# Kernel tuning notes

Hardware: AMD Instinct MI355X
Metric: run time of the kernel (lower is better)

The kernel has to match this reference:

```python
import jax, jax.numpy as jnp
import numpy as np
from jax import lax

T, IN, OUT, E, R = 32768, 2048, 768, 64, 16
SCALING = 32.0 / 16.0  # lora_alpha / r


def setup_inputs() -> dict:
    key = jax.random.key(0)
    k1, k2, k3, k4 = jax.random.split(key, 4)
    x = jax.random.normal(k1, (T, IN), dtype=jnp.float32)
    # Ragged per-expert token counts summing exactly to T (tokens pre-sorted by expert).
    rng = np.random.default_rng(0)
    m_sizes = jnp.asarray(np.bincount(rng.integers(0, E, size=T), minlength=E), dtype=jnp.int32)
    w_base = jax.random.normal(k2, (E, IN, OUT), dtype=jnp.float32) * 0.02
    # NOTE: original inits lora_B to zeros; we use small random values so the
    # LoRA path contributes non-trivially for correctness testing.
    w_a = jax.random.normal(k3, (E, IN, R), dtype=jnp.float32) * (1.0 / np.sqrt(IN))
    w_b = jax.random.normal(k4, (E, R, OUT), dtype=jnp.float32) * 0.02
    return {"x": x, "m_sizes": m_sizes, "w_base": w_base, "w_a": w_a, "w_b": w_b}


def reference(x, m_sizes, w_base, w_a, w_b):
    # Grouped (ragged) GEMM: rows of x are grouped by expert with sizes m_sizes.
    y = lax.ragged_dot(x, w_base, m_sizes)          # [T, OUT] base path
    a = lax.ragged_dot(x, w_a, m_sizes)             # [T, R]   lora_A
    delta = lax.ragged_dot(a, w_b, m_sizes)         # [T, OUT] lora_B
    return y + delta * SCALING
```

## Files before the change

### kernel.cpp

```cpp
#include <hip/hip_runtime.h>

#define TDIM 32768
#define KDIM 2048
#define NDIM 768
#define EDIM 64
#define RDIM 16
#define SCALE 2.0f

#define BM 128
#define BN 128
#define BKE 64
#define PK 40
#define MAXMT 320

typedef __bf16 bf16;
typedef __attribute__((ext_vector_type(8))) __bf16 bf16x8;
typedef __attribute__((ext_vector_type(4))) __bf16 bf16x4;
typedef __attribute__((ext_vector_type(4))) float f32x4;

#define GLOAD16(gp, lp) \
    __builtin_amdgcn_global_load_lds((const __attribute__((address_space(1))) void*)(gp), \
                                     (__attribute__((address_space(3))) void*)(lp), 16, 0, 0)

__global__ __launch_bounds__(256)
void conv_x_k(const float* __restrict__ x, bf16* __restrict__ xb)
{
    size_t i = ((size_t)blockIdx.x * 256 + threadIdx.x) * 8;
    float4 f0 = *reinterpret_cast<const float4*>(x + i);
    float4 f1 = *reinterpret_cast<const float4*>(x + i + 4);
    bf16x8 v;
    v[0] = (bf16)f0.x; v[1] = (bf16)f0.y; v[2] = (bf16)f0.z; v[3] = (bf16)f0.w;
    v[4] = (bf16)f1.x; v[5] = (bf16)f1.y; v[6] = (bf16)f1.z; v[7] = (bf16)f1.w;
    *reinterpret_cast<bf16x8*>(xb + i) = v;
}

__global__ __launch_bounds__(256)
void conv_w_k(const float* __restrict__ w, bf16* __restrict__ wT)
{
    __shared__ bf16 t[32][65];
    const int e  = blockIdx.z;
    const int n0 = blockIdx.x * 32;
    const int k0 = blockIdx.y * 64;
    const float* src = w + (size_t)e * KDIM * NDIM;
    #pragma unroll
    for (int i = 0; i < 8; ++i) {
        int lin = threadIdx.x + i * 256;
        int k = lin >> 5;
        int c = lin & 31;
        t[c][k] = (bf16)src[(size_t)(k0 + k) * NDIM + n0 + c];
    }
    __syncthreads();
    bf16* dst = wT + ((size_t)e * NDIM + n0) * KDIM + k0;
    #pragma unroll
    for (int i = 0; i < 8; ++i) {
        int lin = threadIdx.x + i * 256;
        int n = lin >> 6;
        int k = lin & 63;
        dst[(size_t)n * KDIM + k] = t[n][k];
    }
}

__global__ __launch_bounds__(256)
void prep_small_k(const float* __restrict__ w_a, const int* __restrict__ m_sizes,
                  bf16* __restrict__ waT, int4* __restrict__ tinfo)
{
    if (blockIdx.x < 16) {
        __shared__ bf16 t[RDIM][132];
        const int e  = blockIdx.y;
        const int k0 = blockIdx.x * 128;
        const float* src = w_a + ((size_t)e * KDIM + k0) * RDIM;
        #pragma unroll
        for (int i = 0; i < 8; ++i) {
            int lin = threadIdx.x + i * 256;
            int k = lin >> 4, r = lin & 15;
            t[r][k] = (bf16)src[lin];
        }
        __syncthreads();
        bf16* dst = waT + (size_t)e * RDIM * KDIM + k0;
        #pragma unroll
        for (int i = 0; i < 8; ++i) {
            int lin = threadIdx.x + i * 256;
            int r = lin >> 7, k = lin & 127;
            dst[(size_t)r * KDIM + k] = t[r][k];
        }
    } else if (blockIdx.y == 0) {
        for (int i = threadIdx.x; i < MAXMT; i += 256)
            tinfo[i] = make_int4(0, 0, 0, 0);
        __syncthreads();
        if (threadIdx.x < 64) {
            const int lane = threadIdx.x;
            int m  = m_sizes[lane];
            int nt = (m + BM - 1) >> 7;
            int pm = m, pt = nt;
            #pragma unroll
            for (int d = 1; d < 64; d <<= 1) {
                int vm = __shfl_up(pm, d);
                int vt = __shfl_up(pt, d);
                if (lane >= d) { pm += vm; pt += vt; }
            }
            int row0 = pm - m, tb = pt - nt;
            for (int tI = 0; tI < nt; ++tI) {
                int rr = m - (tI << 7); if (rr > BM) rr = BM;
                tinfo[tb + tI] = make_int4(lane, row0 + (tI << 7), rr, 0);
            }
        }
    }
}

__global__ __launch_bounds__(256, 2)
void lora_moe_bf16(const bf16* __restrict__ xb,
                   const bf16* __restrict__ wT,
                   const bf16* __restrict__ waT,
                   const float* __restrict__ w_b,
                   const int4* __restrict__ tinfo,
                   float* __restrict__ out)
{
    __shared__ bf16 As[BM][BKE];
    __shared__ bf16 Bs[BN][BKE];
    __shared__ bf16 WaS[RDIM][BKE];

    const int tid  = threadIdx.x;
    const int lane = tid & 63;
    const int wave = tid >> 6;
    const int wm   = wave >> 1;
    const int wn   = wave & 1;
    const int quad = lane >> 4;
    const int lrow = lane & 15;

    const int4 ti = tinfo[blockIdx.y];
    const int rows = ti.z;
    if (rows == 0) return;
    const int e      = ti.x;
    const int tstart = ti.y;
    const int n0     = blockIdx.x * BN;

    const bf16* a_base  = xb  + (size_t)tstart * KDIM;
    const bf16* b_base  = wT  + ((size_t)e * NDIM + n0) * KDIM;
    const bf16* wa_base = waT + (size_t)e * RDIM * KDIM;
    const float* wbb_e  = w_b + (size_t)e * RDIM * NDIM;

    f32x4 acc[4][4];
    f32x4 accA[4];
    #pragma unroll
    for (int i = 0; i < 4; ++i) {
        accA[i] = (f32x4){0.f, 0.f, 0.f, 0.f};
        #pragma unroll
        for (int j = 0; j < 4; ++j) acc[i][j] = (f32x4){0.f, 0.f, 0.f, 0.f};
    }

    const int lr8 = lane >> 3;
    const int lg  = lane & 7;

    const bf16* agp[4];
    const bf16* bgp[4];
    #pragma unroll
    for (int i = 0; i < 4; ++i) {
        int r  = wave * 32 + i * 8 + lr8;
        int gr = r < rows ? r : rows - 1;
        agp[i] = a_base + (size_t)gr * KDIM + ((lg ^ (r & 7)) << 3);
        bgp[i] = b_base + (size_t)r  * KDIM + ((lg ^ (r & 7)) << 3);
    }
    const bf16* wagp = wa_base + (size_t)(wave * 8 + lr8) * KDIM + ((lg ^ lr8) << 3);

    const int swzr = (lrow & 7) << 4;

    for (int kk = 0; kk < KDIM; kk += BKE) {
        __syncthreads();
        #pragma unroll
        for (int i = 0; i < 4; ++i)
            GLOAD16(agp[i], &As[wave * 32 + i * 8][0]);
        #pragma unroll
        for (int i = 0; i < 4; ++i)
            GLOAD16(bgp[i], &Bs[wave * 32 + i * 8][0]);
        if (wave < 2)
            GLOAD16(wagp, &WaS[wave * 8][0]);
        #pragma unroll
        for (int i = 0; i < 4; ++i) { agp[i] += BKE; bgp[i] += BKE; }
        wagp += BKE;
        __syncthreads();

        #pragma unroll
        for (int kh = 0; kh < 2; ++kh) {
            const int cb = (kh * 64 + quad * 16) ^ swzr;
            bf16x8 af[4];
            #pragma unroll
            for (int i = 0; i < 4; ++i)
                af[i] = *reinterpret_cast<const bf16x8*>(
                            (const char*)&As[wm * 64 + i * 16 + lrow][0] + cb);
            bf16x8 wf = *reinterpret_cast<const bf16x8*>(
                            (const char*)&WaS[lrow][0] + cb);
            #pragma unroll
            for (int j = 0; j < 4; ++j) {
                bf16x8 bfr = *reinterpret_cast<const bf16x8*>(
                                 (const char*)&Bs[wn * 64 + j * 16 + lrow][0] + cb);
                #pragma unroll
                for (int i = 0; i < 4; ++i)
                    acc[i][j] = __builtin_amdgcn_mfma_f32_16x16x32_bf16(af[i], bfr, acc[i][j], 0, 0, 0);
            }
            #pragma unroll
            for (int i = 0; i < 4; ++i)
                accA[i] = __builtin_amdgcn_mfma_f32_16x16x32_bf16(af[i], wf, accA[i], 0, 0, 0);
        }
    }

    __syncthreads();
    if (wn == 0) {
        #pragma unroll
        for (int i = 0; i < 4; ++i) {
            int mrow = wm * 64 + i * 16 + quad * 4;
            #pragma unroll
            for (int r = 0; r < 4; ++r) {
                int row = mrow + r;
                char* p = (char*)&As[row][0] + ((lrow * 2) ^ ((row & 7) << 4));
                *reinterpret_cast<bf16*>(p) = (bf16)(accA[i][r] * SCALE);
            }
        }
    } else {
        #pragma unroll
        for (int i = 0; i < 4; ++i) {
            int mrow = wm * 64 + i * 16 + quad * 4;
            #pragma unroll
            for (int r = 0; r < 4; ++r) {
                int row = mrow + r;
                char* p = (char*)&As[row][0] + ((32 + lrow * 2) ^ ((row & 7) << 4));
                *reinterpret_cast<bf16*>(p) = (bf16)0.f;
            }
        }
    }
    {
        int n  = tid & 127;
        int r0 = (tid >> 7) * 8;
        const float* p = wbb_e + (size_t)r0 * NDIM + n0 + n;
        bf16x8 v;
        #pragma unroll
        for (int u = 0; u < 8; ++u) v[u] = (bf16)p[(size_t)u * NDIM];
        char* q = (char*)&Bs[n][0];
        *reinterpret_cast<bf16x8*>(q + ((r0 * 2) ^ ((n & 7) << 4))) = v;
        bf16x8 z = {};
        *reinterpret_cast<bf16x8*>(q + ((32 + r0 * 2) ^ ((n & 7) << 4))) = z;
    }
    __syncthreads();
    #pragma unroll
    for (int i = 0; i < 4; ++i) {
        const int cb2 = (quad * 16) ^ swzr;
        bf16x8 af2 = *reinterpret_cast<const bf16x8*>(
                         (const char*)&As[wm * 64 + i * 16 + lrow][0] + cb2);
        #pragma unroll
        for (int j = 0; j < 4; ++j) {
            bf16x8 bf2 = *reinterpret_cast<const bf16x8*>(
                             (const char*)&Bs[wn * 64 + j * 16 + lrow][0] + cb2);
            acc[i][j] = __builtin_amdgcn_mfma_f32_16x16x32_bf16(af2, bf2, acc[i][j], 0, 0, 0);
        }
    }

    #pragma unroll
    for (int i = 0; i < 4; ++i) {
        int mbase = wm * 64 + i * 16 + quad * 4;
        #pragma unroll
        for (int j = 0; j < 4; ++j) {
            int col = n0 + wn * 64 + j * 16 + lrow;
            #pragma unroll
            for (int r = 0; r < 4; ++r) {
                int mr = mbase + r;
                if (mr < rows)
                    out[(size_t)(tstart + mr) * NDIM + col] = acc[i][j][r];
            }
        }
    }
}

__global__ __launch_bounds__(256, 2)
void lora_moe_kernel(const float* __restrict__ x,
                     const int* __restrict__ m_sizes,
                     const float* __restrict__ w_base,
                     const float* __restrict__ w_a,
                     const float* __restrict__ w_b,
                     float* __restrict__ out)
{
    __shared__ bf16 As[BM][PK];
    __shared__ bf16 Bs[BN][PK];
    __shared__ bf16 WaS[RDIM][PK];

    const int tid  = threadIdx.x;
    const int lane = tid & 63;
    const int wave = tid >> 6;
    const int wm   = wave >> 1;
    const int wn   = wave & 1;
    const int quad = lane >> 4;
    const int lrow = lane & 15;

    int tile = blockIdx.y;
    int e = -1, tstart = 0, rows = 0;
    {
        int row0 = 0, acc2 = 0;
        for (int i = 0; i < EDIM; ++i) {
            int m = m_sizes[i];
            int nt = (m + BM - 1) >> 7;
            if (tile < acc2 + nt) {
                e = i;
                int lt = tile - acc2;
                tstart = row0 + (lt << 7);
                rows = m - (lt << 7);
                if (rows > BM) rows = BM;
                break;
            }
            acc2 += nt;
            row0 += m;
        }
    }
    if (e < 0) return;

    const int n0 = blockIdx.x * BN;

    const float* wb_e  = w_base + (size_t)e * KDIM * NDIM;
    const float* wa_e  = w_a    + (size_t)e * KDIM * RDIM;
    const float* wbb_e = w_b    + (size_t)e * RDIM * NDIM;

    f32x4 acc[4][4];
    f32x4 accA[4];
    #pragma unroll
    for (int i = 0; i < 4; ++i) {
        accA[i] = (f32x4){0.f, 0.f, 0.f, 0.f};
        #pragma unroll
        for (int j = 0; j < 4; ++j) acc[i][j] = (f32x4){0.f, 0.f, 0.f, 0.f};
    }

    const int arow  = tid >> 1;
    const int akh   = (tid & 1) * 16;
    const int agrow = tstart + (arow < rows ? arow : rows - 1);
    const float* aptr = x + (size_t)agrow * KDIM + akh;

    const int bn  = tid & 127;
    const int bg0 = (tid >> 7) * 4;

    const int war = tid & 15;
    const int wag = tid >> 4;

    for (int kk = 0; kk < KDIM; kk += 32) {
        __syncthreads();
        {
            const float* p = aptr + kk;
            float4 f0 = *reinterpret_cast<const float4*>(p);
            float4 f1 = *reinterpret_cast<const float4*>(p + 4);
            float4 f2 = *reinterpret_cast<const float4*>(p + 8);
            float4 f3 = *reinterpret_cast<const float4*>(p + 12);
            bf16x8 v0, v1;
            v0[0]=(bf16)f0.x; v0[1]=(bf16)f0.y; v0[2]=(bf16)f0.z; v0[3]=(bf16)f0.w;
            v0[4]=(bf16)f1.x; v0[5]=(bf16)f1.y; v0[6]=(bf16)f1.z; v0[7]=(bf16)f1.w;
            v1[0]=(bf16)f2.x; v1[1]=(bf16)f2.y; v1[2]=(bf16)f2.z; v1[3]=(bf16)f2.w;
            v1[4]=(bf16)f3.x; v1[5]=(bf16)f3.y; v1[6]=(bf16)f3.z; v1[7]=(bf16)f3.w;
            *reinterpret_cast<bf16x8*>(&As[arow][akh])     = v0;
            *reinterpret_cast<bf16x8*>(&As[arow][akh + 8]) = v1;
        }
        {
            #pragma unroll
            for (int gi = 0; gi < 4; ++gi) {
                int k = (bg0 + gi) * 4;
                const float* p = wb_e + (size_t)(kk + k) * NDIM + n0 + bn;
                float a0 = p[0];
                float a1 = p[NDIM];
                float a2 = p[2 * NDIM];
                float a3 = p[3 * NDIM];
                bf16x4 v; v[0]=(bf16)a0; v[1]=(bf16)a1; v[2]=(bf16)a2; v[3]=(bf16)a3;
                *reinterpret_cast<bf16x4*>(&Bs[bn][k]) = v;
            }
        }
        if (wag < 8) {
            int k = wag * 4;
            const float* p = wa_e + (size_t)(kk + k) * RDIM + war;
            bf16x4 v;
            v[0]=(bf16)p[0]; v[1]=(bf16)p[RDIM]; v[2]=(bf16)p[2*RDIM]; v[3]=(bf16)p[3*RDIM];
            *reinterpret_cast<bf16x4*>(&WaS[war][k]) = v;
        }
        __syncthreads();
        bf16x8 af[4];
        #pragma unroll
        for (int i = 0; i < 4; ++i)
            af[i] = *reinterpret_cast<const bf16x8*>(&As[wm*64 + i*16 + lrow][quad*8]);
        bf16x8 wf = *reinterpret_cast<const bf16x8*>(&WaS[lrow][quad*8]);
        #pragma unroll
        for (int j = 0; j < 4; ++j) {
            bf16x8 bfr = *reinterpret_cast<const bf16x8*>(&Bs[wn*64 + j*16 + lrow][quad*8]);
            #pragma unroll
            for (int i = 0; i < 4; ++i)
                acc[i][j] = __builtin_amdgcn_mfma_f32_16x16x32_bf16(af[i], bfr, acc[i][j], 0, 0, 0);
        }
        #pragma unroll
        for (int i = 0; i < 4; ++i)
            accA[i] = __builtin_amdgcn_mfma_f32_16x16x32_bf16(af[i], wf, accA[i], 0, 0, 0);
    }

    __syncthreads();
    if (wn == 0) {
        #pragma unroll
        for (int i = 0; i < 4; ++i) {
            int mrow = wm*64 + i*16 + quad*4;
            #pragma unroll
            for (int r = 0; r < 4; ++r)
                As[mrow + r][lrow] = (bf16)(accA[i][r] * SCALE);
        }
    } else {
        #pragma unroll
        for (int i = 0; i < 4; ++i) {
            int mrow = wm*64 + i*16 + quad*4;
            #pragma unroll
            for (int r = 0; r < 4; ++r)
                As[mrow + r][16 + lrow] = (bf16)0.f;
        }
    }
    {
        int n  = tid & 127;
        int r0 = (tid >> 7) * 8;
        const float* p = wbb_e + (size_t)r0 * NDIM + n0 + n;
        bf16x8 v;
        #pragma unroll
        for (int u = 0; u < 8; ++u) v[u] = (bf16)p[(size_t)u * NDIM];
        *reinterpret_cast<bf16x8*>(&Bs[n][r0]) = v;
        bf16x8 z = {};
        *reinterpret_cast<bf16x8*>(&Bs[n][16 + r0]) = z;
    }
    __syncthreads();
    #pragma unroll
    for (int i = 0; i < 4; ++i) {
        bf16x8 af2 = *reinterpret_cast<const bf16x8*>(&As[wm*64 + i*16 + lrow][quad*8]);
        #pragma unroll
        for (int j = 0; j < 4; ++j) {
            bf16x8 bf2 = *reinterpret_cast<const bf16x8*>(&Bs[wn*64 + j*16 + lrow][quad*8]);
            acc[i][j] = __builtin_amdgcn_mfma_f32_16x16x32_bf16(af2, bf2, acc[i][j], 0, 0, 0);
        }
    }

    #pragma unroll
    for (int i = 0; i < 4; ++i) {
        int mbase = wm*64 + i*16 + quad*4;
        #pragma unroll
        for (int j = 0; j < 4; ++j) {
            int col = n0 + wn*64 + j*16 + lrow;
            #pragma unroll
            for (int r = 0; r < 4; ++r) {
                int mr = mbase + r;
                if (mr < rows)
                    out[(size_t)(tstart + mr) * NDIM + col] = acc[i][j][r];
            }
        }
    }
}

extern "C" void kernel_launch(void* const* d_in, const int* in_sizes, int n_in,
                              void* d_out, int out_size, void* d_ws, size_t ws_size,
                              hipStream_t stream) {
    const float* x       = (const float*)d_in[0];
    const int*   m_sizes = (const int*)  d_in[1];
    const float* w_base  = (const float*)d_in[2];
    const float* w_a     = (const float*)d_in[3];
    const float* w_b     = (const float*)d_in[4];
    float* out = (float*)d_out;

    const size_t off_xb  = 0;
    const size_t off_wT  = off_xb  + (size_t)TDIM * KDIM * sizeof(bf16);
    const size_t off_waT = off_wT  + (size_t)EDIM * NDIM * KDIM * sizeof(bf16);
    const size_t off_ti  = off_waT + (size_t)EDIM * RDIM * KDIM * sizeof(bf16);
    const size_t need    = off_ti  + (size_t)MAXMT * sizeof(int4);

    if (ws_size >= need) {
        bf16* xb   = (bf16*)((char*)d_ws + off_xb);
        bf16* wT   = (bf16*)((char*)d_ws + off_wT);
        bf16* waT  = (bf16*)((char*)d_ws + off_waT);
        int4* tinf = (int4*)((char*)d_ws + off_ti);

        conv_x_k<<<(TDIM * KDIM) / (256 * 8), 256, 0, stream>>>(x, xb);
        conv_w_k<<<dim3(NDIM / 32, KDIM / 64, EDIM), 256, 0, stream>>>(w_base, wT);
        prep_small_k<<<dim3(17, EDIM), 256, 0, stream>>>(w_a, m_sizes, waT, tinf);
        lora_moe_bf16<<<dim3(NDIM / BN, MAXMT), 256, 0, stream>>>(xb, wT, waT, w_b, tinf, out);
    } else {
        lora_moe_kernel<<<dim3(NDIM / BN, MAXMT), 256, 0, stream>>>(x, m_sizes, w_base, w_a, w_b, out);
    }
}
```

Before: 987.0 us.

## Vectorize weight transpose, remap workgroups across XCDs, raise occupancy bound

The weight-conversion transpose now reads float4 rows and writes 16-byte bf16x8 columns over 64x64 tiles, where it previously used scalar strided accesses. The GEMM kernel remaps its linear workgroup id so that consecutive ids are spread across the 8 XCDs while tiles sharing an expert's A/B data stay grouped, aiming at better L2 reuse. The launch bound is raised to 4 waves-per-EU, which may force register spills in the MFMA accumulator-heavy kernel.

Result: faster. 941.2 us (-4.6%).

```diff
diff --git a/kernel.cpp b/kernel.cpp
--- a/kernel.cpp
+++ b/kernel.cpp
@@ -12,10 +12,13 @@
 #define BKE 64
 #define PK 40
 #define MAXMT 320
+#define NTILES (NDIM / BN)
+#define NWG (NTILES * MAXMT)
 
 typedef __bf16 bf16;
 typedef __attribute__((ext_vector_type(8))) __bf16 bf16x8;
 typedef __attribute__((ext_vector_type(4))) __bf16 bf16x4;
+typedef __attribute__((ext_vector_type(2))) __bf16 bf16x2;
 typedef __attribute__((ext_vector_type(4))) float f32x4;
 
 #define GLOAD16(gp, lp) \
@@ -37,26 +40,34 @@
 __global__ __launch_bounds__(256)
 void conv_w_k(const float* __restrict__ w, bf16* __restrict__ wT)
 {
-    __shared__ bf16 t[32][65];
+    __shared__ bf16 t[64][66];
     const int e  = blockIdx.z;
-    const int n0 = blockIdx.x * 32;
+    const int n0 = blockIdx.x * 64;
     const int k0 = blockIdx.y * 64;
-    const float* src = w + (size_t)e * KDIM * NDIM;
-    #pragma unroll
-    for (int i = 0; i < 8; ++i) {
+    const float* src = w + (size_t)e * KDIM * NDIM + (size_t)k0 * NDIM + n0;
+    #pragma unroll
+    for (int i = 0; i < 4; ++i) {
         int lin = threadIdx.x + i * 256;
-        int k = lin >> 5;
-        int c = lin & 31;
-        t[c][k] = (bf16)src[(size_t)(k0 + k) * NDIM + n0 + c];
+        int row = lin >> 4;
+        int c4  = lin & 15;
+        float4 f = *reinterpret_cast<const float4*>(src + (size_t)row * NDIM + c4 * 4);
+        bf16x2 v0, v1;
+        v0[0] = (bf16)f.x; v0[1] = (bf16)f.y;
+        v1[0] = (bf16)f.z; v1[1] = (bf16)f.w;
+        *reinterpret_cast<bf16x2*>(&t[row][c4 * 4])     = v0;
+        *reinterpret_cast<bf16x2*>(&t[row][c4 * 4 + 2]) = v1;
     }
     __syncthreads();
     bf16* dst = wT + ((size_t)e * NDIM + n0) * KDIM + k0;
     #pragma unroll
-    for (int i = 0; i < 8; ++i) {
+    for (int i = 0; i < 2; ++i) {
         int lin = threadIdx.x + i * 256;
-        int n = lin >> 6;
-        int k = lin & 63;
-        dst[(size_t)n * KDIM + k] = t[n][k];
+        int n  = lin >> 3;
+        int kc = lin & 7;
+        bf16x8 v;
+        #pragma unroll
+        for (int j = 0; j < 8; ++j) v[j] = t[kc * 8 + j][n];
+        *reinterpret_cast<bf16x8*>(dst + (size_t)n * KDIM + kc * 8) = v;
     }
 }
 
@@ -107,7 +118,7 @@
     }
 }
 
-__global__ __launch_bounds__(256, 2)
+__global__ __launch_bounds__(256, 4)
 void lora_moe_bf16(const bf16* __restrict__ xb,
                    const bf16* __restrict__ wT,
                    const bf16* __restrict__ waT,
@@ -127,12 +138,17 @@
     const int quad = lane >> 4;
     const int lrow = lane & 15;
 
-    const int4 ti = tinfo[blockIdx.y];
+    const int lin   = blockIdx.y * NTILES + blockIdx.x;
+    const int wid   = (lin & 7) * (NWG >> 3) + (lin >> 3);
+    const int mtile = wid / NTILES;
+    const int ntile = wid - mtile * NTILES;
+
+    const int4 ti = tinfo[mtile];
     const int rows = ti.z;
     if (rows == 0) return;
     const int e      = ti.x;
     const int tstart = ti.y;
-    const int n0     = blockIdx.x * BN;
+    const int n0     = ntile * BN;
 
     const bf16* a_base  = xb  + (size_t)tstart * KDIM;
     const bf16* b_base  = wT  + ((size_t)e * NDIM + n0) * KDIM;
@@ -469,10 +485,10 @@
         int4* tinf = (int4*)((char*)d_ws + off_ti);
 
         conv_x_k<<<(TDIM * KDIM) / (256 * 8), 256, 0, stream>>>(x, xb);
-        conv_w_k<<<dim3(NDIM / 32, KDIM / 64, EDIM), 256, 0, stream>>>(w_base, wT);
+        conv_w_k<<<dim3(NDIM / 64, KDIM / 64, EDIM), 256, 0, stream>>>(w_base, wT);
         prep_small_k<<<dim3(17, EDIM), 256, 0, stream>>>(w_a, m_sizes, waT, tinf);
-        lora_moe_bf16<<<dim3(NDIM / BN, MAXMT), 256, 0, stream>>>(xb, wT, waT, w_b, tinf, out);
+        lora_moe_bf16<<<dim3(NTILES, MAXMT), 256, 0, stream>>>(xb, wT, waT, w_b, tinf, out);
     } else {
-        lora_moe_kernel<<<dim3(NDIM / BN, MAXMT), 256, 0, stream>>>(x, m_sizes, w_base, w_a, w_b, out);
-    }
-}
+        lora_moe_kernel<<<dim3(NTILES, MAXMT), 256, 0, stream>>>(x, m_sizes, w_base, w_a, w_b, out);
+    }
+}
```
